# Optimization experiments

Measured on AMD Instinct MI355X. Metric: run time of the kernel, lower is better.

Reference implementation:

```python
import jax, jax.numpy as jnp
import numpy as np

N_PER_GRAPH = 28
E_PER_GRAPH = 56
B = 16384
C = 128
LN_EPS = 1e-5


def setup_inputs() -> dict:
    key = jax.random.key(0)
    k0, k1, k2 = jax.random.split(key, 3)
    N = B * N_PER_GRAPH
    x = jax.random.normal(k0, (N, C), dtype=jnp.float32)
    # graph-local random edges, offset per graph so edge_weights.repeat(B) lines up
    local = jax.random.randint(k1, (2, B * E_PER_GRAPH), 0, N_PER_GRAPH)
    offset = jnp.repeat(jnp.arange(B, dtype=jnp.int64) * N_PER_GRAPH, E_PER_GRAPH)
    edge_index = (local.astype(jnp.int64) + offset[None, :])
    W = jax.random.normal(k2, (C, C), dtype=jnp.float32) * (1.0 / np.sqrt(C))
    bias = jnp.zeros((C,), jnp.float32)
    edge_weights = jnp.ones((E_PER_GRAPH,), jnp.float32)
    gamma = jnp.ones((C,), jnp.float32)
    beta = jnp.zeros((C,), jnp.float32)
    return {"x": x, "edge_index": edge_index, "W": W, "bias": bias,
            "edge_weights": edge_weights, "gamma": gamma, "beta": beta}


def _gcn_conv(x, edge_index, edge_weight, W, bias):
    # PyG GCNConv: linear -> add self loops (w=1) -> sym-normalize -> scatter-add -> +bias
    N = x.shape[0]
    src, dst = edge_index[0], edge_index[1]
    loop = jnp.arange(N, dtype=edge_index.dtype)
    src_f = jnp.concatenate([src, loop])
    dst_f = jnp.concatenate([dst, loop])
    ew_f = jnp.concatenate([edge_weight, jnp.ones((N,), x.dtype)])
    deg = jax.ops.segment_sum(ew_f, dst_f, num_segments=N)
    dinv = jnp.where(deg > 0, jax.lax.rsqrt(deg), 0.0)
    norm = dinv[src_f] * ew_f * dinv[dst_f]          # [E+N]
    h = x @ W                                        # [N, C]
    msg = h[src_f] * norm[:, None]                   # gather + scale
    agg = jax.ops.segment_sum(msg, dst_f, num_segments=N)  # scatter-add
    return agg + bias


def reference(x, edge_index, W, bias, edge_weights, gamma, beta):
    res = x  # in_channels == out_channels -> residual is Identity
    batch_size = x.shape[0] // N_PER_GRAPH
    edge_weight = jnp.tile(edge_weights, batch_size)  # == edge_weights.repeat(B)
    h = _gcn_conv(x, edge_index, edge_weight, W, bias)
    y = h + res
    mu = jnp.mean(y, axis=-1, keepdims=True)
    var = jnp.mean(jnp.square(y - mu), axis=-1, keepdims=True)
    ln = (y - mu) * jax.lax.rsqrt(var + LN_EPS) * gamma + beta
    return jax.nn.relu(ln)
```

## Files before the change

kernel.cpp:

```cpp
#include <hip/hip_runtime.h>

#define EPG 56
#define ROWS 56
#define EDG 112
#define CH 128
#define LDW 136

typedef float f32x4 __attribute__((ext_vector_type(4)));
typedef __bf16 bf16x8 __attribute__((ext_vector_type(8)));
typedef unsigned short u16;
typedef u16 u16x8 __attribute__((ext_vector_type(8)));
typedef u16 u16x4 __attribute__((ext_vector_type(4)));

__device__ __forceinline__ u16 f2bf(float f){
  union { float f; unsigned u; } v; v.f = f;
  unsigned r = (v.u + 0x7fffu + ((v.u >> 16) & 1u)) >> 16;
  return (u16)r;
}
__device__ __forceinline__ float bf2f(u16 h){
  union { unsigned u; float f; } v; v.u = ((unsigned)h) << 16;
  return v.f;
}

__global__ void pack_w(const float* __restrict__ W, u16* __restrict__ wp){
  int d = blockIdx.x * 256 + threadIdx.x;
  int j  = d & 7;
  int l  = (d >> 3) & 63;
  int ks = (d >> 9) & 3;
  int ct = d >> 11;
  int k = ((l >> 4) << 3) + (ks << 5) + j;
  int c = (ct << 4) + (l & 15);
  wp[d] = f2bf(W[k * CH + c]);
}

__global__ __launch_bounds__(256, 4)
void gcn_fused(const float* __restrict__ x, const int* __restrict__ ei,
               const float* __restrict__ W, const float* __restrict__ bias,
               const float* __restrict__ ew, const float* __restrict__ gamma,
               const float* __restrict__ beta, float* __restrict__ out,
               const u16* __restrict__ wpack, int npairs)
{
  __shared__ alignas(16) u16 Hs[ROWS][LDW];
  __shared__ float gbb[3][CH];
  __shared__ float deg[ROWS];
  __shared__ int   cnt[ROWS], cnt2[ROWS], rs[ROWS + 1];
  __shared__ int   c_src[EDG];
  __shared__ float c_nrm[EDG];

  const int tid  = threadIdx.x;
  const int lane = tid & 63;
  const int wv   = tid >> 6;
  const int hi   = lane >> 4;
  const int p    = blockIdx.x;
  const int Etot = npairs * EDG;

  int es = 0, ed = 0; float eww = 0.f;
  if (tid < EDG){
    es  = ei[p * EDG + tid]        - p * ROWS;
    ed  = ei[Etot + p * EDG + tid] - p * ROWS;
    eww = ew[(tid >= EPG) ? (tid - EPG) : tid];
  }
  if (tid < ROWS){ deg[tid] = 1.0f; cnt[tid] = 0; cnt2[tid] = 0; }
  if (tid < CH){
    gbb[0][tid] = gamma[tid]; gbb[1][tid] = beta[tid]; gbb[2][tid] = bias[tid];
  }

  const int arow = 16 * wv + (lane & 15);
  const int rowc = arow < ROWS ? arow : ROWS - 1;
  const float* xp = x + ((size_t)p * ROWS + rowc) * CH + hi * 8;

  f32x4 acc[8];
  {
    bf16x8 afr[4];
#pragma unroll
    for (int ks = 0; ks < 4; ks++){
      f32x4 lo = *(const f32x4*)(xp + ks * 32);
      f32x4 h4 = *(const f32x4*)(xp + ks * 32 + 4);
      u16x8 t;
      t[0] = f2bf(lo[0]); t[1] = f2bf(lo[1]); t[2] = f2bf(lo[2]); t[3] = f2bf(lo[3]);
      t[4] = f2bf(h4[0]); t[5] = f2bf(h4[1]); t[6] = f2bf(h4[2]); t[7] = f2bf(h4[3]);
      afr[ks] = __builtin_bit_cast(bf16x8, t);
    }
#pragma unroll
    for (int ct = 0; ct < 8; ct++){
      acc[ct] = (f32x4){0.f, 0.f, 0.f, 0.f};
#pragma unroll
      for (int ks = 0; ks < 4; ks++){
        u16x8 b;
        if (wpack){
          b = ((const u16x8*)wpack)[((ct << 2) + ks) * 64 + lane];
        } else {
#pragma unroll
          for (int j = 0; j < 8; j++){
            int k = hi * 8 + ks * 32 + j;
            int c = ct * 16 + (lane & 15);
            b[j] = f2bf(W[k * CH + c]);
          }
        }
        acc[ct] = __builtin_amdgcn_mfma_f32_16x16x32_bf16(
                    afr[ks], __builtin_bit_cast(bf16x8, b), acc[ct], 0, 0, 0);
      }
    }
  }

  {
    int r0 = 16 * wv + (hi << 2);
    int cc = lane & 15;
#pragma unroll
    for (int ct = 0; ct < 8; ct++){
#pragma unroll
      for (int r = 0; r < 4; r++){
        int rr = r0 + r;
        if (rr < ROWS) Hs[rr][16 * ct + cc] = f2bf(acc[ct][r]);
      }
    }
  }
  __syncthreads();

  if (tid < EDG){
    atomicAdd(&deg[ed], eww);
    atomicAdd(&cnt[ed], 1);
  }
  __syncthreads();

  if (tid < ROWS) deg[tid] = rsqrtf(deg[tid]);
  if (wv == 0){
    int v = (lane < ROWS) ? cnt[lane] : 0;
#pragma unroll
    for (int off = 1; off < 64; off <<= 1){
      int n = __shfl_up(v, off, 64);
      if (lane >= off) v += n;
    }
    if (lane < ROWS) rs[lane + 1] = v;
    if (lane == 0)   rs[0] = 0;
  }
  __syncthreads();

  if (tid < EDG){
    float nrm = deg[es] * eww * deg[ed];
    int slot = rs[ed] + atomicAdd(&cnt2[ed], 1);
    c_src[slot] = es;
    c_nrm[slot] = nrm;
  }
  __syncthreads();

  const int half = lane >> 5;
  const int l32  = lane & 31;
  const int c0   = l32 * 4;
  for (int rp = wv; rp < ROWS / 2; rp += 4){
    int row = 2 * rp + half;
    float dv = deg[row];
    float d2 = dv * dv;
    size_t gbase = ((size_t)p * ROWS + row) * CH + c0;
    u16x4 hs = *(const u16x4*)&Hs[row][c0];
    f32x4 xr = *(const f32x4*)(x + gbase);
    f32x4 bb = *(const f32x4*)&gbb[2][c0];
    float y0 = bf2f(hs[0]) * d2 + bb[0] + xr[0];
    float y1 = bf2f(hs[1]) * d2 + bb[1] + xr[1];
    float y2 = bf2f(hs[2]) * d2 + bb[2] + xr[2];
    float y3 = bf2f(hs[3]) * d2 + bb[3] + xr[3];
    int s0 = rs[row], s1 = rs[row + 1];
    for (int i = s0; i < s1; i++){
      int sc = c_src[i]; float nm = c_nrm[i];
      u16x4 hv = *(const u16x4*)&Hs[sc][c0];
      y0 += nm * bf2f(hv[0]);
      y1 += nm * bf2f(hv[1]);
      y2 += nm * bf2f(hv[2]);
      y3 += nm * bf2f(hv[3]);
    }
    float sm = y0 + y1 + y2 + y3;
    float sq = y0*y0 + y1*y1 + y2*y2 + y3*y3;
#pragma unroll
    for (int m = 1; m < 32; m <<= 1){
      sm += __shfl_xor(sm, m, 32);
      sq += __shfl_xor(sq, m, 32);
    }
    float mu   = sm * (1.0f / 128.0f);
    float var  = sq * (1.0f / 128.0f) - mu * mu;
    float rstd = rsqrtf(var + 1e-5f);
    f32x4 g4 = *(const f32x4*)&gbb[0][c0];
    f32x4 b4 = *(const f32x4*)&gbb[1][c0];
    f32x4 o;
    o[0] = fmaxf(0.f, (y0 - mu) * rstd * g4[0] + b4[0]);
    o[1] = fmaxf(0.f, (y1 - mu) * rstd * g4[1] + b4[1]);
    o[2] = fmaxf(0.f, (y2 - mu) * rstd * g4[2] + b4[2]);
    o[3] = fmaxf(0.f, (y3 - mu) * rstd * g4[3] + b4[3]);
    *(f32x4*)(out + gbase) = o;
  }
}

extern "C" void kernel_launch(void* const* d_in, const int* in_sizes, int n_in,
                              void* d_out, int out_size, void* d_ws, size_t ws_size,
                              hipStream_t stream)
{
  const float* x     = (const float*)d_in[0];
  const int*   ei    = (const int*)d_in[1];
  const float* W     = (const float*)d_in[2];
  const float* bias  = (const float*)d_in[3];
  const float* ew    = (const float*)d_in[4];
  const float* gamma = (const float*)d_in[5];
  const float* beta  = (const float*)d_in[6];
  float* out = (float*)d_out;

  int N = in_sizes[0] / CH;
  int npairs = N / ROWS;

  u16* wpack = nullptr;
  if (ws_size >= (size_t)(CH * CH * sizeof(u16))){
    wpack = (u16*)d_ws;
    hipLaunchKernelGGL(pack_w, dim3(CH * CH / 256), dim3(256), 0, stream, W, wpack);
  }

  hipLaunchKernelGGL(gcn_fused, dim3(npairs), dim3(256), 0, stream,
                     x, ei, W, bias, ew, gamma, beta, out, wpack, npairs);
}
```

Baseline: 164.4 us.

## Split CSR build into separate kernel and software-pipeline persistent main kernel

Moves the per-graph-pair degree, normalization and CSR construction into a separate build_csr kernel that writes a compact per-pair record to the workspace. The main kernel becomes persistent (grid capped at 2048) and prefetches the next pair's x rows and CSR record into registers while computing the current one. The goal is to hide global load latency and take the atomics and scan work off the GEMM/aggregation path. In exchange it adds an extra launch and a workspace round trip for the CSR data, and it needs a larger workspace or else falls back to the old path.

Measured after the change: 299.4 us. +82.2%, slower.

```diff
diff --git a/kernel.cpp b/kernel.cpp
--- a/kernel.cpp
+++ b/kernel.cpp
@@ -5,6 +5,8 @@
 #define EDG 112
 #define CH 128
 #define LDW 136
+
+#define CSR_WORDS 384
 
 typedef float f32x4 __attribute__((ext_vector_type(4)));
 typedef __bf16 bf16x8 __attribute__((ext_vector_type(8)));
@@ -31,6 +33,194 @@
   int k = ((l >> 4) << 3) + (ks << 5) + j;
   int c = (ct << 4) + (l & 15);
   wp[d] = f2bf(W[k * CH + c]);
+}
+
+__global__ __launch_bounds__(128)
+void build_csr(const int* __restrict__ ei, const float* __restrict__ ew,
+               int* __restrict__ csr, int npairs)
+{
+  __shared__ float deg[ROWS];
+  __shared__ int cnt[ROWS], cnt2[ROWS], rs[ROWS + 1];
+  const int p = blockIdx.x, tid = threadIdx.x;
+  const int Etot = npairs * EDG;
+  int es = 0, ed = 0; float eww = 0.f;
+  if (tid < ROWS){ deg[tid] = 1.0f; cnt[tid] = 0; cnt2[tid] = 0; }
+  __syncthreads();
+  if (tid < EDG){
+    es  = ei[p * EDG + tid]        - p * ROWS;
+    ed  = ei[Etot + p * EDG + tid] - p * ROWS;
+    eww = ew[(tid >= EPG) ? (tid - EPG) : tid];
+    atomicAdd(&deg[ed], eww);
+    atomicAdd(&cnt[ed], 1);
+  }
+  __syncthreads();
+  if (tid < ROWS) deg[tid] = rsqrtf(deg[tid]);
+  if (tid < 64){
+    int v = (tid < ROWS) ? cnt[tid] : 0;
+#pragma unroll
+    for (int off = 1; off < 64; off <<= 1){
+      int n = __shfl_up(v, off, 64);
+      if (tid >= off) v += n;
+    }
+    if (tid < ROWS) rs[tid + 1] = v;
+    if (tid == 0)   rs[0] = 0;
+  }
+  __syncthreads();
+  int* base = csr + (size_t)p * CSR_WORDS;
+  if (tid < EDG){
+    float nrm = deg[es] * eww * deg[ed];
+    int slot = rs[ed] + atomicAdd(&cnt2[ed], 1);
+    base[128 + slot] = es;
+    ((float*)base)[240 + slot] = nrm;
+  }
+  if (tid < ROWS)  ((float*)base)[tid] = deg[tid];
+  if (tid <= ROWS) base[64 + tid] = rs[tid];
+}
+
+__global__ __launch_bounds__(256, 4)
+void gcn_main(const float* __restrict__ x, const float* __restrict__ bias,
+              const float* __restrict__ gamma, const float* __restrict__ beta,
+              float* __restrict__ out, const u16* __restrict__ wpack,
+              const int* __restrict__ csr, int npairs)
+{
+  __shared__ alignas(16) u16 Hs[ROWS][LDW];
+  __shared__ float gbb[3][CH];
+  __shared__ int cls[CSR_WORDS];
+
+  float* dinv = (float*)&cls[0];
+  int*   rsL  = &cls[64];
+  int*   srcL = &cls[128];
+  float* nrmL = (float*)&cls[240];
+
+  const int tid  = threadIdx.x;
+  const int lane = tid & 63;
+  const int wv   = tid >> 6;
+  const int hi   = lane >> 4;
+
+  if (tid < CH){
+    gbb[0][tid] = gamma[tid]; gbb[1][tid] = beta[tid]; gbb[2][tid] = bias[tid];
+  }
+
+  const int arow = 16 * wv + (lane & 15);
+  const int rowc = arow < ROWS ? arow : ROWS - 1;
+  const int xoff = hi * 8;
+
+  f32x4 pf[8];
+  {
+    const float* xp = x + ((size_t)blockIdx.x * ROWS + rowc) * CH + xoff;
+#pragma unroll
+    for (int ks = 0; ks < 4; ks++){
+      pf[2 * ks]     = *(const f32x4*)(xp + ks * 32);
+      pf[2 * ks + 1] = *(const f32x4*)(xp + ks * 32 + 4);
+    }
+  }
+  int cw0, cw1 = 0;
+  {
+    const int* cp = csr + (size_t)blockIdx.x * CSR_WORDS;
+    cw0 = cp[tid];
+    if (tid < CSR_WORDS - 256) cw1 = cp[256 + tid];
+  }
+
+  for (int q = blockIdx.x; q < npairs; q += gridDim.x){
+    const int qn = q + gridDim.x;
+
+    bf16x8 afr[4];
+#pragma unroll
+    for (int ks = 0; ks < 4; ks++){
+      f32x4 lo = pf[2 * ks], h4 = pf[2 * ks + 1];
+      u16x8 t;
+      t[0] = f2bf(lo[0]); t[1] = f2bf(lo[1]); t[2] = f2bf(lo[2]); t[3] = f2bf(lo[3]);
+      t[4] = f2bf(h4[0]); t[5] = f2bf(h4[1]); t[6] = f2bf(h4[2]); t[7] = f2bf(h4[3]);
+      afr[ks] = __builtin_bit_cast(bf16x8, t);
+    }
+    if (qn < npairs){
+      const float* xp = x + ((size_t)qn * ROWS + rowc) * CH + xoff;
+#pragma unroll
+      for (int ks = 0; ks < 4; ks++){
+        pf[2 * ks]     = *(const f32x4*)(xp + ks * 32);
+        pf[2 * ks + 1] = *(const f32x4*)(xp + ks * 32 + 4);
+      }
+    }
+
+    f32x4 acc[8];
+#pragma unroll
+    for (int ct = 0; ct < 8; ct++){
+      acc[ct] = (f32x4){0.f, 0.f, 0.f, 0.f};
+#pragma unroll
+      for (int ks = 0; ks < 4; ks++){
+        u16x8 b = ((const u16x8*)wpack)[((ct << 2) + ks) * 64 + lane];
+        acc[ct] = __builtin_amdgcn_mfma_f32_16x16x32_bf16(
+                    afr[ks], __builtin_bit_cast(bf16x8, b), acc[ct], 0, 0, 0);
+      }
+    }
+
+    __syncthreads();
+
+    {
+      int r0 = 16 * wv + (hi << 2);
+      int cc = lane & 15;
+#pragma unroll
+      for (int ct = 0; ct < 8; ct++){
+#pragma unroll
+        for (int r = 0; r < 4; r++){
+          int rr = r0 + r;
+          if (rr < ROWS) Hs[rr][16 * ct + cc] = f2bf(acc[ct][r]);
+        }
+      }
+    }
+    cls[tid] = cw0;
+    if (tid < CSR_WORDS - 256) cls[256 + tid] = cw1;
+    if (qn < npairs){
+      const int* cp = csr + (size_t)qn * CSR_WORDS;
+      cw0 = cp[tid];
+      if (tid < CSR_WORDS - 256) cw1 = cp[256 + tid];
+    }
+    __syncthreads();
+
+    const int half = lane >> 5;
+    const int l32  = lane & 31;
+    const int c0   = l32 * 4;
+    for (int rp = wv; rp < ROWS / 2; rp += 4){
+      int row = 2 * rp + half;
+      float dv = dinv[row];
+      float d2 = dv * dv;
+      size_t gbase = ((size_t)q * ROWS + row) * CH + c0;
+      u16x4 hs = *(const u16x4*)&Hs[row][c0];
+      f32x4 xr = *(const f32x4*)(x + gbase);
+      f32x4 bb = *(const f32x4*)&gbb[2][c0];
+      float y0 = bf2f(hs[0]) * d2 + bb[0] + xr[0];
+      float y1 = bf2f(hs[1]) * d2 + bb[1] + xr[1];
+      float y2 = bf2f(hs[2]) * d2 + bb[2] + xr[2];
+      float y3 = bf2f(hs[3]) * d2 + bb[3] + xr[3];
+      int s0 = rsL[row], s1 = rsL[row + 1];
+      for (int i = s0; i < s1; i++){
+        int sc = srcL[i]; float nm = nrmL[i];
+        u16x4 hv = *(const u16x4*)&Hs[sc][c0];
+        y0 += nm * bf2f(hv[0]);
+        y1 += nm * bf2f(hv[1]);
+        y2 += nm * bf2f(hv[2]);
+        y3 += nm * bf2f(hv[3]);
+      }
+      float sm = y0 + y1 + y2 + y3;
+      float sq = y0*y0 + y1*y1 + y2*y2 + y3*y3;
+#pragma unroll
+      for (int m = 1; m < 32; m <<= 1){
+        sm += __shfl_xor(sm, m, 32);
+        sq += __shfl_xor(sq, m, 32);
+      }
+      float mu   = sm * (1.0f / 128.0f);
+      float var  = sq * (1.0f / 128.0f) - mu * mu;
+      float rstd = rsqrtf(var + 1e-5f);
+      f32x4 g4 = *(const f32x4*)&gbb[0][c0];
+      f32x4 b4 = *(const f32x4*)&gbb[1][c0];
+      f32x4 o;
+      o[0] = fmaxf(0.f, (y0 - mu) * rstd * g4[0] + b4[0]);
+      o[1] = fmaxf(0.f, (y1 - mu) * rstd * g4[1] + b4[1]);
+      o[2] = fmaxf(0.f, (y2 - mu) * rstd * g4[2] + b4[2]);
+      o[3] = fmaxf(0.f, (y3 - mu) * rstd * g4[3] + b4[3]);
+      *(f32x4*)(out + gbase) = o;
+    }
+  }
 }
 
 __global__ __launch_bounds__(256, 4)
@@ -205,12 +395,24 @@
   int N = in_sizes[0] / CH;
   int npairs = N / ROWS;
 
-  u16* wpack = nullptr;
-  if (ws_size >= (size_t)(CH * CH * sizeof(u16))){
-    wpack = (u16*)d_ws;
+  const size_t wpack_bytes = (size_t)CH * CH * sizeof(u16);
+  const size_t csr_bytes   = (size_t)npairs * CSR_WORDS * 4;
+
+  if (ws_size >= wpack_bytes + csr_bytes){
+    u16* wpack = (u16*)d_ws;
+    int* csr   = (int*)((char*)d_ws + wpack_bytes);
     hipLaunchKernelGGL(pack_w, dim3(CH * CH / 256), dim3(256), 0, stream, W, wpack);
-  }
-
-  hipLaunchKernelGGL(gcn_fused, dim3(npairs), dim3(256), 0, stream,
-                     x, ei, W, bias, ew, gamma, beta, out, wpack, npairs);
-}
+    hipLaunchKernelGGL(build_csr, dim3(npairs), dim3(128), 0, stream, ei, ew, csr, npairs);
+    int grid = npairs < 2048 ? npairs : 2048;
+    hipLaunchKernelGGL(gcn_main, dim3(grid), dim3(256), 0, stream,
+                       x, bias, gamma, beta, out, wpack, csr, npairs);
+  } else {
+    u16* wpack = nullptr;
+    if (ws_size >= wpack_bytes){
+      wpack = (u16*)d_ws;
+      hipLaunchKernelGGL(pack_w, dim3(CH * CH / 256), dim3(256), 0, stream, W, wpack);
+    }
+    hipLaunchKernelGGL(gcn_fused, dim3(npairs), dim3(256), 0, stream,
+                       x, ei, W, bias, ew, gamma, beta, out, wpack, npairs);
+  }
+}
```
